# Kernel optimization log

Hardware: AMD Instinct MI355X
Metric: run time of the kernel (lower is better)

## Reference

```python
import jax, jax.numpy as jnp
import numpy as np

B = 131072
IN_CH, SEQ = 16, 5
EMB = 64
UDIM = 16
E = 16
RANK = 8
NCLS = 10
TOPK = 2
NUSERS = 1000
EPS_LN = 1e-5


def _ln(x, g, b):
    mu = x.mean(-1, keepdims=True)
    var = ((x - mu) ** 2).mean(-1, keepdims=True)
    return (x - mu) * jax.lax.rsqrt(var + EPS_LN) * g + b


def setup_inputs() -> dict:
    key = jax.random.key(0)
    ks = jax.random.split(key, 20)
    s = lambda i, shape, scale=0.05: (jax.random.normal(ks[i], shape, jnp.float32) * scale)
    return {
        "x": jax.random.normal(ks[0], (B, IN_CH, SEQ), jnp.float32),
        "user_ids": jax.random.randint(ks[1], (B,), 0, NUSERS),
        # backbone: fc1 (80->64), fc2 (64->64), LayerNorm
        "bb_w1": s(2, (IN_CH * SEQ, 64)), "bb_b1": jnp.zeros((64,), jnp.float32),
        "bb_w2": s(3, (64, EMB)), "bb_b2": jnp.zeros((EMB,), jnp.float32),
        "bb_g": jnp.ones((EMB,), jnp.float32), "bb_beta": jnp.zeros((EMB,), jnp.float32),
        # bilinear gate
        "gU": s(4, (E, EMB, RANK), 0.02), "gV": s(5, (E, UDIM, RANK), 0.02),
        "gb": jnp.zeros((E,), jnp.float32),
        # experts (stacked): fc1 (emb->emb), LN, fc2 (emb->ncls)
        "e_w1": s(6, (E, EMB, EMB)), "e_b1": jnp.zeros((E, EMB), jnp.float32),
        "e_g": jnp.ones((E, EMB), jnp.float32), "e_beta": jnp.zeros((E, EMB), jnp.float32),
        "e_w2": s(7, (E, EMB, NCLS)), "e_b2": jnp.zeros((E, NCLS), jnp.float32),
        # user embedding table
        "ut": s(8, (NUSERS, UDIM), 1.0),
    }


def reference(x, user_ids, bb_w1, bb_b1, bb_w2, bb_b2, bb_g, bb_beta,
              gU, gV, gb, e_w1, e_b1, e_g, e_beta, e_w2, e_b2, ut):
    gelu = lambda t: jax.nn.gelu(t, approximate=False)
    # backbone
    xf = x.reshape(x.shape[0], -1)                      # [B, 80]
    h = gelu(xf @ bb_w1 + bb_b1)
    h = gelu(h @ bb_w2 + bb_b2)
    h = _ln(h, bb_g, bb_beta)                           # [B, EMB]
    # user embedding lookup
    u = ut[user_ids]                                    # [B, UDIM]
    # bilinear gate
    hU = jnp.einsum('bd,edr->ber', h, gU)
    uV = jnp.einsum('bd,edr->ber', u, gV)
    g = (hU * uV).sum(-1) + gb                          # [B, E]
    w = jax.nn.softmax(g, axis=-1)
    if TOPK and TOPK < E:
        _, idx = jax.lax.top_k(w, TOPK)
        mask = jnp.zeros_like(w).at[jnp.arange(w.shape[0])[:, None], idx].set(1.0)
        wm = w * mask
        w = wm / jnp.maximum(wm.sum(-1, keepdims=True), 1e-9)
    # experts, dense over all E (matches torch stack over ModuleList)
    z = gelu(jnp.einsum('bd,edk->bek', h, e_w1) + e_b1)  # [B, E, EMB]
    z = _ln(z, e_g, e_beta)
    lpe = jnp.einsum('bek,ekc->bec', z, e_w2) + e_b2     # [B, E, NCLS]
    logits = jnp.einsum('be,bec->bc', w, lpe)            # [B, NCLS]
    return logits
```

## Files before the change

### kernel.cpp

```cpp
#include <hip/hip_runtime.h>
#include <math.h>

#define BATCH   131072
#define IN_F    80
#define EMB     64
#define NE      16
#define RANK    8
#define UDIM    16
#define NCLS    10
#define NUSERS  1000

#define OFF_H      0ull
#define OFF_A      33554432ull
#define OFF_TOPE   37650432ull
#define OFF_TOPW   38699008ull
#define OFF_PAIRB  39747584ull
#define OFF_PAIRW  40796160ull
#define OFF_HIST   41844736ull
#define OFF_OFFS   41845760ull
#define OFF_CUR    41846784ull

__device__ __forceinline__ float gelu_f(float v) {
    return 0.5f * v * (1.0f + erff(v * 0.70710678118654752440f));
}
__device__ __forceinline__ float4 gelu4(float4 v) {
    v.x = gelu_f(v.x); v.y = gelu_f(v.y); v.z = gelu_f(v.z); v.w = gelu_f(v.w);
    return v;
}
__device__ __forceinline__ float4 sfma4(float s, float4 w, float4 a) {
    a.x = fmaf(s, w.x, a.x); a.y = fmaf(s, w.y, a.y);
    a.z = fmaf(s, w.z, a.z); a.w = fmaf(s, w.w, a.w);
    return a;
}
__device__ __forceinline__ float4 ffma4(float4 v, float4 w, float4 a) {
    a.x = fmaf(v.x, w.x, a.x); a.y = fmaf(v.y, w.y, a.y);
    a.z = fmaf(v.z, w.z, a.z); a.w = fmaf(v.w, w.w, a.w);
    return a;
}
__device__ __forceinline__ float4 add4(float4 a, float4 b) {
    a.x += b.x; a.y += b.y; a.z += b.z; a.w += b.w; return a;
}
__device__ __forceinline__ float4 ln4(float4 z, float mu, float inv, float4 g, float4 bb) {
    float4 r;
    r.x = fmaf((z.x - mu) * inv, g.x, bb.x);
    r.y = fmaf((z.y - mu) * inv, g.y, bb.y);
    r.z = fmaf((z.z - mu) * inv, g.z, bb.z);
    r.w = fmaf((z.w - mu) * inv, g.w, bb.w);
    return r;
}
__device__ __forceinline__ float4 shflx4(float4 a, int m) {
    float4 r;
    r.x = __shfl_xor(a.x, m, 64); r.y = __shfl_xor(a.y, m, 64);
    r.z = __shfl_xor(a.z, m, 64); r.w = __shfl_xor(a.w, m, 64);
    return r;
}

#define FMA16Z(S, WB) do { \
    z0 = sfma4((S), (WB)[0],  z0); z1 = sfma4((S), (WB)[1],  z1); \
    z2 = sfma4((S), (WB)[2],  z2); z3 = sfma4((S), (WB)[3],  z3); \
    z4 = sfma4((S), (WB)[4],  z4); z5 = sfma4((S), (WB)[5],  z5); \
    z6 = sfma4((S), (WB)[6],  z6); z7 = sfma4((S), (WB)[7],  z7); \
    z8 = sfma4((S), (WB)[8],  z8); z9 = sfma4((S), (WB)[9],  z9); \
    za = sfma4((S), (WB)[10], za); zb = sfma4((S), (WB)[11], zb); \
    zc = sfma4((S), (WB)[12], zc); zd = sfma4((S), (WB)[13], zd); \
    ze = sfma4((S), (WB)[14], ze); zf = sfma4((S), (WB)[15], zf); } while (0)

__global__ void k_prep(const float* __restrict__ gU, const float* __restrict__ gV,
                       const float* __restrict__ ut, float* __restrict__ A)
{
    int idx = blockIdx.x * 256 + threadIdx.x;
    if (idx >= NUSERS * NE) return;
    int u = idx / NE, e = idx - u * NE;

    const float4* up = (const float4*)(ut + (size_t)u * UDIM);
    float4 u0 = up[0], u1 = up[1], u2 = up[2], u3 = up[3];

    float4 va = make_float4(0.f, 0.f, 0.f, 0.f);
    float4 vb = make_float4(0.f, 0.f, 0.f, 0.f);
    const float4* gv4 = (const float4*)gV;
#define UVSTEP(UD, DD) do { \
        float4 g0 = gv4[(e * UDIM + (DD)) * 2 + 0]; \
        float4 g1 = gv4[(e * UDIM + (DD)) * 2 + 1]; \
        va = sfma4((UD), g0, va); vb = sfma4((UD), g1, vb); } while (0)
    UVSTEP(u0.x, 0);  UVSTEP(u0.y, 1);  UVSTEP(u0.z, 2);  UVSTEP(u0.w, 3);
    UVSTEP(u1.x, 4);  UVSTEP(u1.y, 5);  UVSTEP(u1.z, 6);  UVSTEP(u1.w, 7);
    UVSTEP(u2.x, 8);  UVSTEP(u2.y, 9);  UVSTEP(u2.z, 10); UVSTEP(u2.w, 11);
    UVSTEP(u3.x, 12); UVSTEP(u3.y, 13); UVSTEP(u3.z, 14); UVSTEP(u3.w, 15);
#undef UVSTEP

    const float4* gu4 = (const float4*)gU;
    float* Ao = A + ((size_t)u * NE + e) * EMB;
    for (int d = 0; d < EMB; ++d) {
        float4 q0 = gu4[(e * EMB + d) * 2 + 0];
        float4 q1 = gu4[(e * EMB + d) * 2 + 1];
        float a = 0.0f;
        a = fmaf(q0.x, va.x, a); a = fmaf(q0.y, va.y, a);
        a = fmaf(q0.z, va.z, a); a = fmaf(q0.w, va.w, a);
        a = fmaf(q1.x, vb.x, a); a = fmaf(q1.y, vb.y, a);
        a = fmaf(q1.z, vb.z, a); a = fmaf(q1.w, vb.w, a);
        Ao[d] = a;
    }
}

__global__ __launch_bounds__(256) void k_fc1(
    const float* __restrict__ x,
    const float* __restrict__ w1, const float* __restrict__ b1,
    float* __restrict__ h1_out)
{
    __shared__ __align__(16) float4 s_w1[IN_F * 16];
    __shared__ __align__(16) float4 s_b1[16];

    const int tid = threadIdx.x;
    {
        const float4* g1 = (const float4*)w1;
        for (int i = tid; i < IN_F * 16; i += 256) s_w1[i] = g1[i];
        if (tid < 16) s_b1[tid] = ((const float4*)b1)[tid];
    }
    __syncthreads();

    const int b = blockIdx.x * 256 + tid;
    const float4* xp = (const float4*)(x + (size_t)b * IN_F);

    float4 z0 = s_b1[0],  z1 = s_b1[1],  z2 = s_b1[2],  z3 = s_b1[3];
    float4 z4 = s_b1[4],  z5 = s_b1[5],  z6 = s_b1[6],  z7 = s_b1[7];
    float4 z8 = s_b1[8],  z9 = s_b1[9],  za = s_b1[10], zb = s_b1[11];
    float4 zc = s_b1[12], zd = s_b1[13], ze = s_b1[14], zf = s_b1[15];

#pragma unroll 1
    for (int t = 0; t < 5; ++t) {
        float4 xA = xp[4*t+0], xB = xp[4*t+1], xC = xp[4*t+2], xD = xp[4*t+3];
        const float4* wr = s_w1 + (t * 16) * 16;
        FMA16Z(xA.x, wr);       FMA16Z(xA.y, wr + 16);  FMA16Z(xA.z, wr + 32);  FMA16Z(xA.w, wr + 48);
        FMA16Z(xB.x, wr + 64);  FMA16Z(xB.y, wr + 80);  FMA16Z(xB.z, wr + 96);  FMA16Z(xB.w, wr + 112);
        FMA16Z(xC.x, wr + 128); FMA16Z(xC.y, wr + 144); FMA16Z(xC.z, wr + 160); FMA16Z(xC.w, wr + 176);
        FMA16Z(xD.x, wr + 192); FMA16Z(xD.y, wr + 208); FMA16Z(xD.z, wr + 224); FMA16Z(xD.w, wr + 240);
    }
    z0 = gelu4(z0); z1 = gelu4(z1); z2 = gelu4(z2); z3 = gelu4(z3);
    z4 = gelu4(z4); z5 = gelu4(z5); z6 = gelu4(z6); z7 = gelu4(z7);
    z8 = gelu4(z8); z9 = gelu4(z9); za = gelu4(za); zb = gelu4(zb);
    zc = gelu4(zc); zd = gelu4(zd); ze = gelu4(ze); zf = gelu4(zf);

    float4* ho = (float4*)(h1_out + (size_t)b * EMB);
    ho[0] = z0;  ho[1] = z1;  ho[2] = z2;  ho[3] = z3;
    ho[4] = z4;  ho[5] = z5;  ho[6] = z6;  ho[7] = z7;
    ho[8] = z8;  ho[9] = z9;  ho[10] = za; ho[11] = zb;
    ho[12] = zc; ho[13] = zd; ho[14] = ze; ho[15] = zf;
}

__global__ __launch_bounds__(256) void k_fc2gate(
    float* h,
    const int* __restrict__ uid,
    const float* __restrict__ w2, const float* __restrict__ b2,
    const float* __restrict__ gam, const float* __restrict__ bet,
    const float* __restrict__ A, const float* __restrict__ gb,
    int* __restrict__ top_e, float* __restrict__ top_w, int* __restrict__ hist)
{
    __shared__ __align__(16) float4 s_w2[EMB * 16];
    __shared__ __align__(16) float4 s_b2[16], s_ga[16], s_be[16];
    __shared__ float s_gb[NE];
    __shared__ int s_hist[NE];

    const int tid = threadIdx.x;
    {
        const float4* g2 = (const float4*)w2;
        for (int i = tid; i < EMB * 16; i += 256) s_w2[i] = g2[i];
        if (tid < 16) {
            s_b2[tid] = ((const float4*)b2)[tid];
            s_ga[tid] = ((const float4*)gam)[tid];
            s_be[tid] = ((const float4*)bet)[tid];
        }
        if (tid < NE) { s_gb[tid] = gb[tid]; s_hist[tid] = 0; }
    }
    __syncthreads();

    const int b = blockIdx.x * 256 + tid;
    float4* hp = (float4*)(h + (size_t)b * EMB);

    float4 z0 = s_b2[0],  z1 = s_b2[1],  z2 = s_b2[2],  z3 = s_b2[3];
    float4 z4 = s_b2[4],  z5 = s_b2[5],  z6 = s_b2[6],  z7 = s_b2[7];
    float4 z8 = s_b2[8],  z9 = s_b2[9],  za = s_b2[10], zb = s_b2[11];
    float4 zc = s_b2[12], zd = s_b2[13], ze = s_b2[14], zf = s_b2[15];
#pragma unroll 1
    for (int t = 0; t < 4; ++t) {
        float4 hA = hp[4*t+0], hB = hp[4*t+1], hC = hp[4*t+2], hD = hp[4*t+3];
        const float4* wr = s_w2 + (t * 16) * 16;
        FMA16Z(hA.x, wr);       FMA16Z(hA.y, wr + 16);  FMA16Z(hA.z, wr + 32);  FMA16Z(hA.w, wr + 48);
        FMA16Z(hB.x, wr + 64);  FMA16Z(hB.y, wr + 80);  FMA16Z(hB.z, wr + 96);  FMA16Z(hB.w, wr + 112);
        FMA16Z(hC.x, wr + 128); FMA16Z(hC.y, wr + 144); FMA16Z(hC.z, wr + 160); FMA16Z(hC.w, wr + 176);
        FMA16Z(hD.x, wr + 192); FMA16Z(hD.y, wr + 208); FMA16Z(hD.z, wr + 224); FMA16Z(hD.w, wr + 240);
    }
    z0 = gelu4(z0); z1 = gelu4(z1); z2 = gelu4(z2); z3 = gelu4(z3);
    z4 = gelu4(z4); z5 = gelu4(z5); z6 = gelu4(z6); z7 = gelu4(z7);
    z8 = gelu4(z8); z9 = gelu4(z9); za = gelu4(za); zb = gelu4(zb);
    zc = gelu4(zc); zd = gelu4(zd); ze = gelu4(ze); zf = gelu4(zf);

    float4 sA = add4(add4(add4(z0, z1), add4(z2, z3)), add4(add4(z4, z5), add4(z6, z7)));
    float4 sB = add4(add4(add4(z8, z9), add4(za, zb)), add4(add4(zc, zd), add4(ze, zf)));
    float4 sS = add4(sA, sB);
    float mu = (sS.x + sS.y + sS.z + sS.w) * (1.0f / 64.0f);
    float4 vv = make_float4(0.f, 0.f, 0.f, 0.f);
#define BBV(Z) do { float4 d4; d4.x = (Z).x - mu; d4.y = (Z).y - mu; d4.z = (Z).z - mu; d4.w = (Z).w - mu; \
                    vv = ffma4(d4, d4, vv); } while (0)
    BBV(z0); BBV(z1); BBV(z2); BBV(z3); BBV(z4); BBV(z5); BBV(z6); BBV(z7);
    BBV(z8); BBV(z9); BBV(za); BBV(zb); BBV(zc); BBV(zd); BBV(ze); BBV(zf);
#undef BBV
    float var = (vv.x + vv.y + vv.z + vv.w) * (1.0f / 64.0f);
    float inv = 1.0f / sqrtf(var + 1e-5f);
    z0 = ln4(z0, mu, inv, s_ga[0],  s_be[0]);
    z1 = ln4(z1, mu, inv, s_ga[1],  s_be[1]);
    z2 = ln4(z2, mu, inv, s_ga[2],  s_be[2]);
    z3 = ln4(z3, mu, inv, s_ga[3],  s_be[3]);
    z4 = ln4(z4, mu, inv, s_ga[4],  s_be[4]);
    z5 = ln4(z5, mu, inv, s_ga[5],  s_be[5]);
    z6 = ln4(z6, mu, inv, s_ga[6],  s_be[6]);
    z7 = ln4(z7, mu, inv, s_ga[7],  s_be[7]);
    z8 = ln4(z8, mu, inv, s_ga[8],  s_be[8]);
    z9 = ln4(z9, mu, inv, s_ga[9],  s_be[9]);
    za = ln4(za, mu, inv, s_ga[10], s_be[10]);
    zb = ln4(zb, mu, inv, s_ga[11], s_be[11]);
    zc = ln4(zc, mu, inv, s_ga[12], s_be[12]);
    zd = ln4(zd, mu, inv, s_ga[13], s_be[13]);
    ze = ln4(ze, mu, inv, s_ga[14], s_be[14]);
    zf = ln4(zf, mu, inv, s_ga[15], s_be[15]);

    hp[0] = z0;  hp[1] = z1;  hp[2] = z2;  hp[3] = z3;
    hp[4] = z4;  hp[5] = z5;  hp[6] = z6;  hp[7] = z7;
    hp[8] = z8;  hp[9] = z9;  hp[10] = za; hp[11] = zb;
    hp[12] = zc; hp[13] = zd; hp[14] = ze; hp[15] = zf;

    const int u = uid[b];
    const float4* Ap = (const float4*)(A + (size_t)u * NE * EMB);
    float m0 = -1e30f, m1 = -1e30f;
    int i0 = 0, i1 = 0;
#pragma unroll 1
    for (int e = 0; e < NE; ++e) {
        const float4* ap = Ap + e * 16;
        float4 ac = make_float4(0.f, 0.f, 0.f, 0.f);
        ac = ffma4(z0, ap[0],  ac); ac = ffma4(z1, ap[1],  ac);
        ac = ffma4(z2, ap[2],  ac); ac = ffma4(z3, ap[3],  ac);
        ac = ffma4(z4, ap[4],  ac); ac = ffma4(z5, ap[5],  ac);
        ac = ffma4(z6, ap[6],  ac); ac = ffma4(z7, ap[7],  ac);
        ac = ffma4(z8, ap[8],  ac); ac = ffma4(z9, ap[9],  ac);
        ac = ffma4(za, ap[10], ac); ac = ffma4(zb, ap[11], ac);
        ac = ffma4(zc, ap[12], ac); ac = ffma4(zd, ap[13], ac);
        ac = ffma4(ze, ap[14], ac); ac = ffma4(zf, ap[15], ac);
        float ge = ((ac.x + ac.y) + (ac.z + ac.w)) + s_gb[e];
        if (ge > m0)      { m1 = m0; i1 = i0; m0 = ge; i0 = e; }
        else if (ge > m1) { m1 = ge; i1 = e; }
    }
    float t = expf(m1 - m0);
    float w0n = 1.0f / (1.0f + t);
    float w1n = t / (1.0f + t);

    top_e[2*b+0] = i0; top_w[2*b+0] = w0n;
    top_e[2*b+1] = i1; top_w[2*b+1] = w1n;
    atomicAdd(&s_hist[i0], 1);
    atomicAdd(&s_hist[i1], 1);
    __syncthreads();
    if (tid < NE) atomicAdd(&hist[tid], s_hist[tid]);
}

__global__ void k_scan(const int* __restrict__ hist, int* __restrict__ offs, int* __restrict__ cur)
{
    if (blockIdx.x == 0 && threadIdx.x == 0) {
        int acc = 0;
        for (int e = 0; e < NE; ++e) { offs[e] = acc; cur[e] = acc; acc += hist[e]; }
    }
}

__global__ __launch_bounds__(256) void k_scatter(
    const int* __restrict__ top_e, const float* __restrict__ top_w,
    int* __restrict__ cur, int* __restrict__ pair_b, float* __restrict__ pair_w)
{
    __shared__ int lh[NE];
    __shared__ int lbase[NE];
    const int tid = threadIdx.x;
    if (tid < NE) lh[tid] = 0;
    __syncthreads();

    const int b = blockIdx.x * 256 + tid;
    const int e0 = top_e[2*b+0];
    const int e1 = top_e[2*b+1];
    atomicAdd(&lh[e0], 1);
    atomicAdd(&lh[e1], 1);
    __syncthreads();
    if (tid < NE) {
        lbase[tid] = atomicAdd(&cur[tid], lh[tid]);
        lh[tid] = 0;
    }
    __syncthreads();
    int r0 = atomicAdd(&lh[e0], 1);
    int p0 = lbase[e0] + r0;
    pair_b[p0] = b; pair_w[p0] = top_w[2*b+0];
    int r1 = atomicAdd(&lh[e1], 1);
    int p1 = lbase[e1] + r1;
    pair_b[p1] = b; pair_w[p1] = top_w[2*b+1];
}

#define EXP_BX 128
__global__ __launch_bounds__(256, 2) void k_expert(
    const float* __restrict__ h,
    const int* __restrict__ pair_b, const float* __restrict__ pair_w,
    const int* __restrict__ hist, const int* __restrict__ offs,
    const float* __restrict__ ew1, const float* __restrict__ eb1,
    const float* __restrict__ eg, const float* __restrict__ ebeta,
    const float* __restrict__ ew2, const float* __restrict__ eb2,
    float* __restrict__ out)
{
    const int e = blockIdx.y;
    const int cnt = hist[e];
    if ((int)(blockIdx.x * 64) >= cnt) return;

    __shared__ __align__(16) float4 s_w1[EMB * 16];
    __shared__ __align__(16) float4 s_w2[EMB * 3];
    __shared__ __align__(16) float4 s_b1[16], s_ga[16], s_be[16], s_b2[3];

    const int tid = threadIdx.x;
    {
        const float4* g1 = (const float4*)(ew1 + (size_t)e * EMB * EMB);
        for (int i = tid; i < EMB * 16; i += 256) s_w1[i] = g1[i];
        float* w2f = (float*)s_w2;
        for (int i = tid; i < EMB * 12; i += 256) {
            int k = i / 12, c = i - k * 12;
            w2f[i] = (c < NCLS) ? ew2[((size_t)e * EMB + k) * NCLS + c] : 0.0f;
        }
        if (tid < 16) {
            s_b1[tid] = ((const float4*)(eb1   + (size_t)e * EMB))[tid];
            s_ga[tid] = ((const float4*)(eg    + (size_t)e * EMB))[tid];
            s_be[tid] = ((const float4*)(ebeta + (size_t)e * EMB))[tid];
        }
        float* b2f = (float*)s_b2;
        if (tid < 12) b2f[tid] = (tid < NCLS) ? eb2[e * NCLS + tid] : 0.0f;
    }
    __syncthreads();

    const int base = offs[e];
    const int q  = tid & 3;
    const int pl = tid >> 2;

    for (int p0 = blockIdx.x * 64; p0 < cnt; p0 += EXP_BX * 64) {
        const int pr = p0 + pl;
        if (pr >= cnt) continue;
        const int idx = base + pr;
        const int b = pair_b[idx];
        const float pw = pair_w[idx];

        const float4* hp = (const float4*)(h + (size_t)b * EMB);

        float4 z0 = s_b1[q*4+0], z1 = s_b1[q*4+1], z2 = s_b1[q*4+2], z3 = s_b1[q*4+3];
#define FMA4Q(S, WB) do { \
        z0 = sfma4((S), (WB)[0], z0); z1 = sfma4((S), (WB)[1], z1); \
        z2 = sfma4((S), (WB)[2], z2); z3 = sfma4((S), (WB)[3], z3); } while (0)
#pragma unroll 1
        for (int t = 0; t < 4; ++t) {
            float4 hA = hp[4*t+0], hB = hp[4*t+1], hC = hp[4*t+2], hD = hp[4*t+3];
            const float4* wr = s_w1 + (t * 16) * 16 + q * 4;
            FMA4Q(hA.x, wr + 0*16);  FMA4Q(hA.y, wr + 1*16);  FMA4Q(hA.z, wr + 2*16);  FMA4Q(hA.w, wr + 3*16);
            FMA4Q(hB.x, wr + 4*16);  FMA4Q(hB.y, wr + 5*16);  FMA4Q(hB.z, wr + 6*16);  FMA4Q(hB.w, wr + 7*16);
            FMA4Q(hC.x, wr + 8*16);  FMA4Q(hC.y, wr + 9*16);  FMA4Q(hC.z, wr + 10*16); FMA4Q(hC.w, wr + 11*16);
            FMA4Q(hD.x, wr + 12*16); FMA4Q(hD.y, wr + 13*16); FMA4Q(hD.z, wr + 14*16); FMA4Q(hD.w, wr + 15*16);
        }
#undef FMA4Q
        z0 = gelu4(z0); z1 = gelu4(z1); z2 = gelu4(z2); z3 = gelu4(z3);

        float4 sA = add4(add4(z0, z1), add4(z2, z3));
        float sl = (sA.x + sA.y) + (sA.z + sA.w);
        sl += __shfl_xor(sl, 1, 64);
        sl += __shfl_xor(sl, 2, 64);
        float mu = sl * (1.0f / 64.0f);

        float4 vv = make_float4(0.f, 0.f, 0.f, 0.f);
#define EXV(Z) do { float4 d4; d4.x = (Z).x - mu; d4.y = (Z).y - mu; d4.z = (Z).z - mu; d4.w = (Z).w - mu; \
                    vv = ffma4(d4, d4, vv); } while (0)
        EXV(z0); EXV(z1); EXV(z2); EXV(z3);
#undef EXV
        float vl = (vv.x + vv.y) + (vv.z + vv.w);
        vl += __shfl_xor(vl, 1, 64);
        vl += __shfl_xor(vl, 2, 64);
        float var = vl * (1.0f / 64.0f);
        float inv = 1.0f / sqrtf(var + 1e-5f);

        z0 = ln4(z0, mu, inv, s_ga[q*4+0], s_be[q*4+0]);
        z1 = ln4(z1, mu, inv, s_ga[q*4+1], s_be[q*4+1]);
        z2 = ln4(z2, mu, inv, s_ga[q*4+2], s_be[q*4+2]);
        z3 = ln4(z3, mu, inv, s_ga[q*4+3], s_be[q*4+3]);

        float4 a0 = make_float4(0.f, 0.f, 0.f, 0.f);
        float4 a1 = make_float4(0.f, 0.f, 0.f, 0.f);
        float4 a2 = make_float4(0.f, 0.f, 0.f, 0.f);
#define EXF2(S, I) do { \
        const float4* wr = s_w2 + (q * 16 + (I)) * 3; \
        a0 = sfma4((S), wr[0], a0); a1 = sfma4((S), wr[1], a1); a2 = sfma4((S), wr[2], a2); } while (0)
        EXF2(z0.x, 0);  EXF2(z0.y, 1);  EXF2(z0.z, 2);  EXF2(z0.w, 3);
        EXF2(z1.x, 4);  EXF2(z1.y, 5);  EXF2(z1.z, 6);  EXF2(z1.w, 7);
        EXF2(z2.x, 8);  EXF2(z2.y, 9);  EXF2(z2.z, 10); EXF2(z2.w, 11);
        EXF2(z3.x, 12); EXF2(z3.y, 13); EXF2(z3.z, 14); EXF2(z3.w, 15);
#undef EXF2

        a0 = add4(a0, shflx4(a0, 1)); a0 = add4(a0, shflx4(a0, 2));
        a1 = add4(a1, shflx4(a1, 1)); a1 = add4(a1, shflx4(a1, 2));
        a2 = add4(a2, shflx4(a2, 1)); a2 = add4(a2, shflx4(a2, 2));

        if (q == 0) {
            a0 = add4(a0, s_b2[0]); a1 = add4(a1, s_b2[1]); a2 = add4(a2, s_b2[2]);
            float* ob = out + (size_t)b * NCLS;
            atomicAdd(ob + 0, pw * a0.x);
            atomicAdd(ob + 1, pw * a0.y);
            atomicAdd(ob + 2, pw * a0.z);
            atomicAdd(ob + 3, pw * a0.w);
            atomicAdd(ob + 4, pw * a1.x);
            atomicAdd(ob + 5, pw * a1.y);
            atomicAdd(ob + 6, pw * a1.z);
            atomicAdd(ob + 7, pw * a1.w);
            atomicAdd(ob + 8, pw * a2.x);
            atomicAdd(ob + 9, pw * a2.y);
        }
    }
}

extern "C" void kernel_launch(void* const* d_in, const int* in_sizes, int n_in,
                              void* d_out, int out_size, void* d_ws, size_t ws_size,
                              hipStream_t stream)
{
    (void)in_sizes; (void)n_in; (void)out_size; (void)ws_size;

    const float* x     = (const float*)d_in[0];
    const int*   uid   = (const int*)  d_in[1];
    const float* bb_w1 = (const float*)d_in[2];
    const float* bb_b1 = (const float*)d_in[3];
    const float* bb_w2 = (const float*)d_in[4];
    const float* bb_b2 = (const float*)d_in[5];
    const float* bb_g  = (const float*)d_in[6];
    const float* bb_be = (const float*)d_in[7];
    const float* gU    = (const float*)d_in[8];
    const float* gV    = (const float*)d_in[9];
    const float* gb    = (const float*)d_in[10];
    const float* e_w1  = (const float*)d_in[11];
    const float* e_b1  = (const float*)d_in[12];
    const float* e_g   = (const float*)d_in[13];
    const float* e_be  = (const float*)d_in[14];
    const float* e_w2  = (const float*)d_in[15];
    const float* e_b2  = (const float*)d_in[16];
    const float* ut    = (const float*)d_in[17];

    float* out = (float*)d_out;
    char*  ws  = (char*)d_ws;

    float* h      = (float*)(ws + OFF_H);
    float* A      = (float*)(ws + OFF_A);
    int*   top_e  = (int*)  (ws + OFF_TOPE);
    float* top_w  = (float*)(ws + OFF_TOPW);
    int*   pair_b = (int*)  (ws + OFF_PAIRB);
    float* pair_w = (float*)(ws + OFF_PAIRW);
    int*   hist   = (int*)  (ws + OFF_HIST);
    int*   offs   = (int*)  (ws + OFF_OFFS);
    int*   cur    = (int*)  (ws + OFF_CUR);

    hipMemsetAsync(out, 0, (size_t)BATCH * NCLS * sizeof(float), stream);
    hipMemsetAsync(hist, 0, NE * sizeof(int), stream);

    k_prep<<<(NUSERS * NE + 255) / 256, 256, 0, stream>>>(gU, gV, ut, A);
    k_fc1<<<BATCH / 256, 256, 0, stream>>>(x, bb_w1, bb_b1, h);
    k_fc2gate<<<BATCH / 256, 256, 0, stream>>>(h, uid, bb_w2, bb_b2, bb_g, bb_be,
                                               A, gb, top_e, top_w, hist);
    k_scan<<<1, 64, 0, stream>>>(hist, offs, cur);
    k_scatter<<<BATCH / 256, 256, 0, stream>>>(top_e, top_w, cur, pair_b, pair_w);
    dim3 eg(EXP_BX, NE);
    k_expert<<<eg, 256, 0, stream>>>(h, pair_b, pair_w, hist, offs,
                                     e_w1, e_b1, e_g, e_be, e_w2, e_b2, out);
}
```

Before: 384.3 us.

## Split rows across 4 lanes with 2 rows per thread in fc1, fc2gate, expert

Restructures the backbone fc1 and fc2+gate kernels so each group of four lanes shares two batch rows, with each lane computing a quarter of the output columns. LayerNorm statistics and the gate dot products are reduced with shuffles. The expert kernel now processes two pairs per lane group and uses a padded per-quarter w2 layout in shared memory. The aim is lower register pressure, so that two blocks fit per CU, and reuse of each shared-memory weight load across two rows. The cost is extra shuffle reductions and redundant per-row loads of h/x across lanes.

```diff
diff --git a/kernel.cpp b/kernel.cpp
--- a/kernel.cpp
+++ b/kernel.cpp
@@ -55,15 +55,13 @@
     return r;
 }
 
-#define FMA16Z(S, WB) do { \
-    z0 = sfma4((S), (WB)[0],  z0); z1 = sfma4((S), (WB)[1],  z1); \
-    z2 = sfma4((S), (WB)[2],  z2); z3 = sfma4((S), (WB)[3],  z3); \
-    z4 = sfma4((S), (WB)[4],  z4); z5 = sfma4((S), (WB)[5],  z5); \
-    z6 = sfma4((S), (WB)[6],  z6); z7 = sfma4((S), (WB)[7],  z7); \
-    z8 = sfma4((S), (WB)[8],  z8); z9 = sfma4((S), (WB)[9],  z9); \
-    za = sfma4((S), (WB)[10], za); zb = sfma4((S), (WB)[11], zb); \
-    zc = sfma4((S), (WB)[12], zc); zd = sfma4((S), (WB)[13], zd); \
-    ze = sfma4((S), (WB)[14], ze); zf = sfma4((S), (WB)[15], zf); } while (0)
+#define FMAD2(SA, SB) do { \
+    float4 w0_ = wr[0], w1_ = wr[1], w2_ = wr[2], w3_ = wr[3]; \
+    zA0 = sfma4((SA), w0_, zA0); zA1 = sfma4((SA), w1_, zA1); \
+    zA2 = sfma4((SA), w2_, zA2); zA3 = sfma4((SA), w3_, zA3); \
+    zB0 = sfma4((SB), w0_, zB0); zB1 = sfma4((SB), w1_, zB1); \
+    zB2 = sfma4((SB), w2_, zB2); zB3 = sfma4((SB), w3_, zB3); \
+    wr += 16; } while (0)
 
 __global__ void k_prep(const float* __restrict__ gU, const float* __restrict__ gV,
                        const float* __restrict__ ut, float* __restrict__ A)
@@ -102,7 +100,7 @@
     }
 }
 
-__global__ __launch_bounds__(256) void k_fc1(
+__global__ __launch_bounds__(256, 2) void k_fc1(
     const float* __restrict__ x,
     const float* __restrict__ w1, const float* __restrict__ b1,
     float* __restrict__ h1_out)
@@ -118,36 +116,34 @@
     }
     __syncthreads();
 
-    const int b = blockIdx.x * 256 + tid;
-    const float4* xp = (const float4*)(x + (size_t)b * IN_F);
-
-    float4 z0 = s_b1[0],  z1 = s_b1[1],  z2 = s_b1[2],  z3 = s_b1[3];
-    float4 z4 = s_b1[4],  z5 = s_b1[5],  z6 = s_b1[6],  z7 = s_b1[7];
-    float4 z8 = s_b1[8],  z9 = s_b1[9],  za = s_b1[10], zb = s_b1[11];
-    float4 zc = s_b1[12], zd = s_b1[13], ze = s_b1[14], zf = s_b1[15];
+    const int q  = tid & 3;
+    const int pl = tid >> 2;
+    const int bA = blockIdx.x * 128 + 2 * pl;
+    const int bB = bA + 1;
+    const float4* xpA = (const float4*)(x + (size_t)bA * IN_F);
+    const float4* xpB = (const float4*)(x + (size_t)bB * IN_F);
+
+    float4 zA0 = s_b1[q*4+0], zA1 = s_b1[q*4+1], zA2 = s_b1[q*4+2], zA3 = s_b1[q*4+3];
+    float4 zB0 = zA0, zB1 = zA1, zB2 = zA2, zB3 = zA3;
 
 #pragma unroll 1
-    for (int t = 0; t < 5; ++t) {
-        float4 xA = xp[4*t+0], xB = xp[4*t+1], xC = xp[4*t+2], xD = xp[4*t+3];
-        const float4* wr = s_w1 + (t * 16) * 16;
-        FMA16Z(xA.x, wr);       FMA16Z(xA.y, wr + 16);  FMA16Z(xA.z, wr + 32);  FMA16Z(xA.w, wr + 48);
-        FMA16Z(xB.x, wr + 64);  FMA16Z(xB.y, wr + 80);  FMA16Z(xB.z, wr + 96);  FMA16Z(xB.w, wr + 112);
-        FMA16Z(xC.x, wr + 128); FMA16Z(xC.y, wr + 144); FMA16Z(xC.z, wr + 160); FMA16Z(xC.w, wr + 176);
-        FMA16Z(xD.x, wr + 192); FMA16Z(xD.y, wr + 208); FMA16Z(xD.z, wr + 224); FMA16Z(xD.w, wr + 240);
-    }
-    z0 = gelu4(z0); z1 = gelu4(z1); z2 = gelu4(z2); z3 = gelu4(z3);
-    z4 = gelu4(z4); z5 = gelu4(z5); z6 = gelu4(z6); z7 = gelu4(z7);
-    z8 = gelu4(z8); z9 = gelu4(z9); za = gelu4(za); zb = gelu4(zb);
-    zc = gelu4(zc); zd = gelu4(zd); ze = gelu4(ze); zf = gelu4(zf);
-
-    float4* ho = (float4*)(h1_out + (size_t)b * EMB);
-    ho[0] = z0;  ho[1] = z1;  ho[2] = z2;  ho[3] = z3;
-    ho[4] = z4;  ho[5] = z5;  ho[6] = z6;  ho[7] = z7;
-    ho[8] = z8;  ho[9] = z9;  ho[10] = za; ho[11] = zb;
-    ho[12] = zc; ho[13] = zd; ho[14] = ze; ho[15] = zf;
-}
-
-__global__ __launch_bounds__(256) void k_fc2gate(
+    for (int t = 0; t < 10; ++t) {
+        float4 a0 = xpA[2*t+0], a1 = xpA[2*t+1];
+        float4 b0 = xpB[2*t+0], b1 = xpB[2*t+1];
+        const float4* wr = s_w1 + (8*t) * 16 + q * 4;
+        FMAD2(a0.x, b0.x); FMAD2(a0.y, b0.y); FMAD2(a0.z, b0.z); FMAD2(a0.w, b0.w);
+        FMAD2(a1.x, b1.x); FMAD2(a1.y, b1.y); FMAD2(a1.z, b1.z); FMAD2(a1.w, b1.w);
+    }
+    zA0 = gelu4(zA0); zA1 = gelu4(zA1); zA2 = gelu4(zA2); zA3 = gelu4(zA3);
+    zB0 = gelu4(zB0); zB1 = gelu4(zB1); zB2 = gelu4(zB2); zB3 = gelu4(zB3);
+
+    float4* hoA = (float4*)(h1_out + (size_t)bA * EMB);
+    float4* hoB = (float4*)(h1_out + (size_t)bB * EMB);
+    hoA[q*4+0] = zA0; hoA[q*4+1] = zA1; hoA[q*4+2] = zA2; hoA[q*4+3] = zA3;
+    hoB[q*4+0] = zB0; hoB[q*4+1] = zB1; hoB[q*4+2] = zB2; hoB[q*4+3] = zB3;
+}
+
+__global__ __launch_bounds__(256, 2) void k_fc2gate(
     float* h,
     const int* __restrict__ uid,
     const float* __restrict__ w2, const float* __restrict__ b2,
@@ -173,89 +169,119 @@
     }
     __syncthreads();
 
-    const int b = blockIdx.x * 256 + tid;
-    float4* hp = (float4*)(h + (size_t)b * EMB);
-
-    float4 z0 = s_b2[0],  z1 = s_b2[1],  z2 = s_b2[2],  z3 = s_b2[3];
-    float4 z4 = s_b2[4],  z5 = s_b2[5],  z6 = s_b2[6],  z7 = s_b2[7];
-    float4 z8 = s_b2[8],  z9 = s_b2[9],  za = s_b2[10], zb = s_b2[11];
-    float4 zc = s_b2[12], zd = s_b2[13], ze = s_b2[14], zf = s_b2[15];
+    const int q  = tid & 3;
+    const int pl = tid >> 2;
+    const int bA = blockIdx.x * 128 + 2 * pl;
+    const int bB = bA + 1;
+    float4* hpA = (float4*)(h + (size_t)bA * EMB);
+    float4* hpB = (float4*)(h + (size_t)bB * EMB);
+
+    float4 zA0 = s_b2[q*4+0], zA1 = s_b2[q*4+1], zA2 = s_b2[q*4+2], zA3 = s_b2[q*4+3];
+    float4 zB0 = zA0, zB1 = zA1, zB2 = zA2, zB3 = zA3;
+
 #pragma unroll 1
-    for (int t = 0; t < 4; ++t) {
-        float4 hA = hp[4*t+0], hB = hp[4*t+1], hC = hp[4*t+2], hD = hp[4*t+3];
-        const float4* wr = s_w2 + (t * 16) * 16;
-        FMA16Z(hA.x, wr);       FMA16Z(hA.y, wr + 16);  FMA16Z(hA.z, wr + 32);  FMA16Z(hA.w, wr + 48);
-        FMA16Z(hB.x, wr + 64);  FMA16Z(hB.y, wr + 80);  FMA16Z(hB.z, wr + 96);  FMA16Z(hB.w, wr + 112);
-        FMA16Z(hC.x, wr + 128); FMA16Z(hC.y, wr + 144); FMA16Z(hC.z, wr + 160); FMA16Z(hC.w, wr + 176);
-        FMA16Z(hD.x, wr + 192); FMA16Z(hD.y, wr + 208); FMA16Z(hD.z, wr + 224); FMA16Z(hD.w, wr + 240);
-    }
-    z0 = gelu4(z0); z1 = gelu4(z1); z2 = gelu4(z2); z3 = gelu4(z3);
-    z4 = gelu4(z4); z5 = gelu4(z5); z6 = gelu4(z6); z7 = gelu4(z7);
-    z8 = gelu4(z8); z9 = gelu4(z9); za = gelu4(za); zb = gelu4(zb);
-    zc = gelu4(zc); zd = gelu4(zd); ze = gelu4(ze); zf = gelu4(zf);
-
-    float4 sA = add4(add4(add4(z0, z1), add4(z2, z3)), add4(add4(z4, z5), add4(z6, z7)));
-    float4 sB = add4(add4(add4(z8, z9), add4(za, zb)), add4(add4(zc, zd), add4(ze, zf)));
-    float4 sS = add4(sA, sB);
-    float mu = (sS.x + sS.y + sS.z + sS.w) * (1.0f / 64.0f);
-    float4 vv = make_float4(0.f, 0.f, 0.f, 0.f);
-#define BBV(Z) do { float4 d4; d4.x = (Z).x - mu; d4.y = (Z).y - mu; d4.z = (Z).z - mu; d4.w = (Z).w - mu; \
-                    vv = ffma4(d4, d4, vv); } while (0)
-    BBV(z0); BBV(z1); BBV(z2); BBV(z3); BBV(z4); BBV(z5); BBV(z6); BBV(z7);
-    BBV(z8); BBV(z9); BBV(za); BBV(zb); BBV(zc); BBV(zd); BBV(ze); BBV(zf);
-#undef BBV
-    float var = (vv.x + vv.y + vv.z + vv.w) * (1.0f / 64.0f);
-    float inv = 1.0f / sqrtf(var + 1e-5f);
-    z0 = ln4(z0, mu, inv, s_ga[0],  s_be[0]);
-    z1 = ln4(z1, mu, inv, s_ga[1],  s_be[1]);
-    z2 = ln4(z2, mu, inv, s_ga[2],  s_be[2]);
-    z3 = ln4(z3, mu, inv, s_ga[3],  s_be[3]);
-    z4 = ln4(z4, mu, inv, s_ga[4],  s_be[4]);
-    z5 = ln4(z5, mu, inv, s_ga[5],  s_be[5]);
-    z6 = ln4(z6, mu, inv, s_ga[6],  s_be[6]);
-    z7 = ln4(z7, mu, inv, s_ga[7],  s_be[7]);
-    z8 = ln4(z8, mu, inv, s_ga[8],  s_be[8]);
-    z9 = ln4(z9, mu, inv, s_ga[9],  s_be[9]);
-    za = ln4(za, mu, inv, s_ga[10], s_be[10]);
-    zb = ln4(zb, mu, inv, s_ga[11], s_be[11]);
-    zc = ln4(zc, mu, inv, s_ga[12], s_be[12]);
-    zd = ln4(zd, mu, inv, s_ga[13], s_be[13]);
-    ze = ln4(ze, mu, inv, s_ga[14], s_be[14]);
-    zf = ln4(zf, mu, inv, s_ga[15], s_be[15]);
-
-    hp[0] = z0;  hp[1] = z1;  hp[2] = z2;  hp[3] = z3;
-    hp[4] = z4;  hp[5] = z5;  hp[6] = z6;  hp[7] = z7;
-    hp[8] = z8;  hp[9] = z9;  hp[10] = za; hp[11] = zb;
-    hp[12] = zc; hp[13] = zd; hp[14] = ze; hp[15] = zf;
-
-    const int u = uid[b];
-    const float4* Ap = (const float4*)(A + (size_t)u * NE * EMB);
-    float m0 = -1e30f, m1 = -1e30f;
-    int i0 = 0, i1 = 0;
-#pragma unroll 1
-    for (int e = 0; e < NE; ++e) {
-        const float4* ap = Ap + e * 16;
-        float4 ac = make_float4(0.f, 0.f, 0.f, 0.f);
-        ac = ffma4(z0, ap[0],  ac); ac = ffma4(z1, ap[1],  ac);
-        ac = ffma4(z2, ap[2],  ac); ac = ffma4(z3, ap[3],  ac);
-        ac = ffma4(z4, ap[4],  ac); ac = ffma4(z5, ap[5],  ac);
-        ac = ffma4(z6, ap[6],  ac); ac = ffma4(z7, ap[7],  ac);
-        ac = ffma4(z8, ap[8],  ac); ac = ffma4(z9, ap[9],  ac);
-        ac = ffma4(za, ap[10], ac); ac = ffma4(zb, ap[11], ac);
-        ac = ffma4(zc, ap[12], ac); ac = ffma4(zd, ap[13], ac);
-        ac = ffma4(ze, ap[14], ac); ac = ffma4(zf, ap[15], ac);
-        float ge = ((ac.x + ac.y) + (ac.z + ac.w)) + s_gb[e];
-        if (ge > m0)      { m1 = m0; i1 = i0; m0 = ge; i0 = e; }
-        else if (ge > m1) { m1 = ge; i1 = e; }
-    }
-    float t = expf(m1 - m0);
-    float w0n = 1.0f / (1.0f + t);
-    float w1n = t / (1.0f + t);
-
-    top_e[2*b+0] = i0; top_w[2*b+0] = w0n;
-    top_e[2*b+1] = i1; top_w[2*b+1] = w1n;
-    atomicAdd(&s_hist[i0], 1);
-    atomicAdd(&s_hist[i1], 1);
+    for (int t = 0; t < 8; ++t) {
+        float4 a0 = hpA[2*t+0], a1 = hpA[2*t+1];
+        float4 b0 = hpB[2*t+0], b1 = hpB[2*t+1];
+        const float4* wr = s_w2 + (8*t) * 16 + q * 4;
+        FMAD2(a0.x, b0.x); FMAD2(a0.y, b0.y); FMAD2(a0.z, b0.z); FMAD2(a0.w, b0.w);
+        FMAD2(a1.x, b1.x); FMAD2(a1.y, b1.y); FMAD2(a1.z, b1.z); FMAD2(a1.w, b1.w);
+    }
+    zA0 = gelu4(zA0); zA1 = gelu4(zA1); zA2 = gelu4(zA2); zA3 = gelu4(zA3);
+    zB0 = gelu4(zB0); zB1 = gelu4(zB1); zB2 = gelu4(zB2); zB3 = gelu4(zB3);
+
+    float4 sA4 = add4(add4(zA0, zA1), add4(zA2, zA3));
+    float slA = (sA4.x + sA4.y) + (sA4.z + sA4.w);
+    slA += __shfl_xor(slA, 1, 64); slA += __shfl_xor(slA, 2, 64);
+    float muA = slA * (1.0f / 64.0f);
+    float4 sB4 = add4(add4(zB0, zB1), add4(zB2, zB3));
+    float slB = (sB4.x + sB4.y) + (sB4.z + sB4.w);
+    slB += __shfl_xor(slB, 1, 64); slB += __shfl_xor(slB, 2, 64);
+    float muB = slB * (1.0f / 64.0f);
+
+    float4 vvA = make_float4(0.f, 0.f, 0.f, 0.f);
+    float4 vvB = make_float4(0.f, 0.f, 0.f, 0.f);
+#define VACC(V, Z, MU) do { float4 d4; d4.x = (Z).x - (MU); d4.y = (Z).y - (MU); \
+        d4.z = (Z).z - (MU); d4.w = (Z).w - (MU); V = ffma4(d4, d4, V); } while (0)
+    VACC(vvA, zA0, muA); VACC(vvA, zA1, muA); VACC(vvA, zA2, muA); VACC(vvA, zA3, muA);
+    VACC(vvB, zB0, muB); VACC(vvB, zB1, muB); VACC(vvB, zB2, muB); VACC(vvB, zB3, muB);
+#undef VACC
+    float vlA = (vvA.x + vvA.y) + (vvA.z + vvA.w);
+    vlA += __shfl_xor(vlA, 1, 64); vlA += __shfl_xor(vlA, 2, 64);
+    float invA = 1.0f / sqrtf(vlA * (1.0f / 64.0f) + 1e-5f);
+    float vlB = (vvB.x + vvB.y) + (vvB.z + vvB.w);
+    vlB += __shfl_xor(vlB, 1, 64); vlB += __shfl_xor(vlB, 2, 64);
+    float invB = 1.0f / sqrtf(vlB * (1.0f / 64.0f) + 1e-5f);
+
+    zA0 = ln4(zA0, muA, invA, s_ga[q*4+0], s_be[q*4+0]);
+    zA1 = ln4(zA1, muA, invA, s_ga[q*4+1], s_be[q*4+1]);
+    zA2 = ln4(zA2, muA, invA, s_ga[q*4+2], s_be[q*4+2]);
+    zA3 = ln4(zA3, muA, invA, s_ga[q*4+3], s_be[q*4+3]);
+    zB0 = ln4(zB0, muB, invB, s_ga[q*4+0], s_be[q*4+0]);
+    zB1 = ln4(zB1, muB, invB, s_ga[q*4+1], s_be[q*4+1]);
+    zB2 = ln4(zB2, muB, invB, s_ga[q*4+2], s_be[q*4+2]);
+    zB3 = ln4(zB3, muB, invB, s_ga[q*4+3], s_be[q*4+3]);
+
+    hpA[q*4+0] = zA0; hpA[q*4+1] = zA1; hpA[q*4+2] = zA2; hpA[q*4+3] = zA3;
+    hpB[q*4+0] = zB0; hpB[q*4+1] = zB1; hpB[q*4+2] = zB2; hpB[q*4+3] = zB3;
+
+    const int uA = uid[bA], uB = uid[bB];
+    const float* AbA = A + (size_t)uA * NE * EMB + q * 16;
+    const float* AbB = A + (size_t)uB * NE * EMB + q * 16;
+    float gA0,gA1,gA2,gA3,gA4,gA5,gA6,gA7,gA8,gA9,gAa,gAb,gAc,gAd,gAe,gAf;
+    float gB0,gB1,gB2,gB3,gB4,gB5,gB6,gB7,gB8,gB9,gBa,gBb,gBc,gBd,gBe,gBf;
+#define GDOT(GV, AB, E, Z0, Z1, Z2, Z3) do { \
+    const float4* ap = (const float4*)((AB) + (E) * EMB); \
+    float4 ac = make_float4(0.f, 0.f, 0.f, 0.f); \
+    ac = ffma4(Z0, ap[0], ac); ac = ffma4(Z1, ap[1], ac); \
+    ac = ffma4(Z2, ap[2], ac); ac = ffma4(Z3, ap[3], ac); \
+    GV = (ac.x + ac.y) + (ac.z + ac.w); \
+    GV += __shfl_xor(GV, 1, 64); GV += __shfl_xor(GV, 2, 64); \
+    GV += s_gb[(E)]; } while (0)
+    GDOT(gA0, AbA, 0,  zA0,zA1,zA2,zA3); GDOT(gA1, AbA, 1,  zA0,zA1,zA2,zA3);
+    GDOT(gA2, AbA, 2,  zA0,zA1,zA2,zA3); GDOT(gA3, AbA, 3,  zA0,zA1,zA2,zA3);
+    GDOT(gA4, AbA, 4,  zA0,zA1,zA2,zA3); GDOT(gA5, AbA, 5,  zA0,zA1,zA2,zA3);
+    GDOT(gA6, AbA, 6,  zA0,zA1,zA2,zA3); GDOT(gA7, AbA, 7,  zA0,zA1,zA2,zA3);
+    GDOT(gA8, AbA, 8,  zA0,zA1,zA2,zA3); GDOT(gA9, AbA, 9,  zA0,zA1,zA2,zA3);
+    GDOT(gAa, AbA, 10, zA0,zA1,zA2,zA3); GDOT(gAb, AbA, 11, zA0,zA1,zA2,zA3);
+    GDOT(gAc, AbA, 12, zA0,zA1,zA2,zA3); GDOT(gAd, AbA, 13, zA0,zA1,zA2,zA3);
+    GDOT(gAe, AbA, 14, zA0,zA1,zA2,zA3); GDOT(gAf, AbA, 15, zA0,zA1,zA2,zA3);
+    GDOT(gB0, AbB, 0,  zB0,zB1,zB2,zB3); GDOT(gB1, AbB, 1,  zB0,zB1,zB2,zB3);
+    GDOT(gB2, AbB, 2,  zB0,zB1,zB2,zB3); GDOT(gB3, AbB, 3,  zB0,zB1,zB2,zB3);
+    GDOT(gB4, AbB, 4,  zB0,zB1,zB2,zB3); GDOT(gB5, AbB, 5,  zB0,zB1,zB2,zB3);
+    GDOT(gB6, AbB, 6,  zB0,zB1,zB2,zB3); GDOT(gB7, AbB, 7,  zB0,zB1,zB2,zB3);
+    GDOT(gB8, AbB, 8,  zB0,zB1,zB2,zB3); GDOT(gB9, AbB, 9,  zB0,zB1,zB2,zB3);
+    GDOT(gBa, AbB, 10, zB0,zB1,zB2,zB3); GDOT(gBb, AbB, 11, zB0,zB1,zB2,zB3);
+    GDOT(gBc, AbB, 12, zB0,zB1,zB2,zB3); GDOT(gBd, AbB, 13, zB0,zB1,zB2,zB3);
+    GDOT(gBe, AbB, 14, zB0,zB1,zB2,zB3); GDOT(gBf, AbB, 15, zB0,zB1,zB2,zB3);
+#undef GDOT
+
+#define T2(G, E) do { float gv_ = (G); \
+    if (gv_ > m0) { m1 = m0; i1 = i0; m0 = gv_; i0 = (E); } \
+    else if (gv_ > m1) { m1 = gv_; i1 = (E); } } while (0)
+    if (q == 0) {
+        {
+            float m0 = -1e30f, m1 = -1e30f; int i0 = 0, i1 = 0;
+            T2(gA0,0); T2(gA1,1); T2(gA2,2); T2(gA3,3); T2(gA4,4); T2(gA5,5);
+            T2(gA6,6); T2(gA7,7); T2(gA8,8); T2(gA9,9); T2(gAa,10); T2(gAb,11);
+            T2(gAc,12); T2(gAd,13); T2(gAe,14); T2(gAf,15);
+            float t = expf(m1 - m0);
+            top_e[2*bA+0] = i0; top_w[2*bA+0] = 1.0f / (1.0f + t);
+            top_e[2*bA+1] = i1; top_w[2*bA+1] = t / (1.0f + t);
+            atomicAdd(&s_hist[i0], 1); atomicAdd(&s_hist[i1], 1);
+        }
+        {
+            float m0 = -1e30f, m1 = -1e30f; int i0 = 0, i1 = 0;
+            T2(gB0,0); T2(gB1,1); T2(gB2,2); T2(gB3,3); T2(gB4,4); T2(gB5,5);
+            T2(gB6,6); T2(gB7,7); T2(gB8,8); T2(gB9,9); T2(gBa,10); T2(gBb,11);
+            T2(gBc,12); T2(gBd,13); T2(gBe,14); T2(gBf,15);
+            float t = expf(m1 - m0);
+            top_e[2*bB+0] = i0; top_w[2*bB+0] = 1.0f / (1.0f + t);
+            top_e[2*bB+1] = i1; top_w[2*bB+1] = t / (1.0f + t);
+            atomicAdd(&s_hist[i0], 1); atomicAdd(&s_hist[i1], 1);
+        }
+    }
+#undef T2
     __syncthreads();
     if (tid < NE) atomicAdd(&hist[tid], s_hist[tid]);
 }
@@ -309,111 +335,141 @@
 {
     const int e = blockIdx.y;
     const int cnt = hist[e];
-    if ((int)(blockIdx.x * 64) >= cnt) return;
+    if ((int)(blockIdx.x * 128) >= cnt) return;
 
     __shared__ __align__(16) float4 s_w1[EMB * 16];
-    __shared__ __align__(16) float4 s_w2[EMB * 3];
-    __shared__ __align__(16) float4 s_b1[16], s_ga[16], s_be[16], s_b2[3];
+    __shared__ __align__(16) float4 s_w2q[4 * 52];
+    __shared__ __align__(16) float4 s_b1[16], s_ga[16], s_be[16];
+    __shared__ float s_b2s[12];
 
     const int tid = threadIdx.x;
     {
         const float4* g1 = (const float4*)(ew1 + (size_t)e * EMB * EMB);
         for (int i = tid; i < EMB * 16; i += 256) s_w1[i] = g1[i];
-        float* w2f = (float*)s_w2;
-        for (int i = tid; i < EMB * 12; i += 256) {
-            int k = i / 12, c = i - k * 12;
-            w2f[i] = (c < NCLS) ? ew2[((size_t)e * EMB + k) * NCLS + c] : 0.0f;
+        float* w2f = (float*)s_w2q;
+        for (int i = tid; i < 4 * 192; i += 256) {
+            int cp = i / 192, r = i - cp * 192;
+            int k = r / 12, c = r - k * 12;
+            w2f[cp * 208 + r] = (c < NCLS)
+                ? ew2[((size_t)e * EMB + cp * 16 + k) * NCLS + c] : 0.0f;
         }
         if (tid < 16) {
             s_b1[tid] = ((const float4*)(eb1   + (size_t)e * EMB))[tid];
             s_ga[tid] = ((const float4*)(eg    + (size_t)e * EMB))[tid];
             s_be[tid] = ((const float4*)(ebeta + (size_t)e * EMB))[tid];
         }
-        float* b2f = (float*)s_b2;
-        if (tid < 12) b2f[tid] = (tid < NCLS) ? eb2[e * NCLS + tid] : 0.0f;
+        if (tid < 12) s_b2s[tid] = (tid < NCLS) ? eb2[e * NCLS + tid] : 0.0f;
     }
     __syncthreads();
 
     const int base = offs[e];
     const int q  = tid & 3;
     const int pl = tid >> 2;
-
-    for (int p0 = blockIdx.x * 64; p0 < cnt; p0 += EXP_BX * 64) {
-        const int pr = p0 + pl;
-        if (pr >= cnt) continue;
-        const int idx = base + pr;
-        const int b = pair_b[idx];
-        const float pw = pair_w[idx];
-
-        const float4* hp = (const float4*)(h + (size_t)b * EMB);
-
-        float4 z0 = s_b1[q*4+0], z1 = s_b1[q*4+1], z2 = s_b1[q*4+2], z3 = s_b1[q*4+3];
-#define FMA4Q(S, WB) do { \
-        z0 = sfma4((S), (WB)[0], z0); z1 = sfma4((S), (WB)[1], z1); \
-        z2 = sfma4((S), (WB)[2], z2); z3 = sfma4((S), (WB)[3], z3); } while (0)
+    const float4* w2r = s_w2q + q * 52;
+
+    for (int p0 = blockIdx.x * 128; p0 < cnt; p0 += EXP_BX * 128) {
+        const int prA = p0 + 2 * pl;
+        if (prA >= cnt) continue;
+        const int prB = prA + 1;
+        const bool vB = (prB < cnt);
+        const int idxA = base + prA;
+        const int idxB = base + (vB ? prB : prA);
+        const int bA = pair_b[idxA], bB = pair_b[idxB];
+        const float pwA = pair_w[idxA], pwB = pair_w[idxB];
+
+        const float4* hpA = (const float4*)(h + (size_t)bA * EMB);
+        const float4* hpB = (const float4*)(h + (size_t)bB * EMB);
+
+        float4 zA0 = s_b1[q*4+0], zA1 = s_b1[q*4+1], zA2 = s_b1[q*4+2], zA3 = s_b1[q*4+3];
+        float4 zB0 = zA0, zB1 = zA1, zB2 = zA2, zB3 = zA3;
 #pragma unroll 1
-        for (int t = 0; t < 4; ++t) {
-            float4 hA = hp[4*t+0], hB = hp[4*t+1], hC = hp[4*t+2], hD = hp[4*t+3];
-            const float4* wr = s_w1 + (t * 16) * 16 + q * 4;
-            FMA4Q(hA.x, wr + 0*16);  FMA4Q(hA.y, wr + 1*16);  FMA4Q(hA.z, wr + 2*16);  FMA4Q(hA.w, wr + 3*16);
-            FMA4Q(hB.x, wr + 4*16);  FMA4Q(hB.y, wr + 5*16);  FMA4Q(hB.z, wr + 6*16);  FMA4Q(hB.w, wr + 7*16);
-            FMA4Q(hC.x, wr + 8*16);  FMA4Q(hC.y, wr + 9*16);  FMA4Q(hC.z, wr + 10*16); FMA4Q(hC.w, wr + 11*16);
-            FMA4Q(hD.x, wr + 12*16); FMA4Q(hD.y, wr + 13*16); FMA4Q(hD.z, wr + 14*16); FMA4Q(hD.w, wr + 15*16);
-        }
-#undef FMA4Q
-        z0 = gelu4(z0); z1 = gelu4(z1); z2 = gelu4(z2); z3 = gelu4(z3);
-
-        float4 sA = add4(add4(z0, z1), add4(z2, z3));
-        float sl = (sA.x + sA.y) + (sA.z + sA.w);
-        sl += __shfl_xor(sl, 1, 64);
-        sl += __shfl_xor(sl, 2, 64);
-        float mu = sl * (1.0f / 64.0f);
-
-        float4 vv = make_float4(0.f, 0.f, 0.f, 0.f);
-#define EXV(Z) do { float4 d4; d4.x = (Z).x - mu; d4.y = (Z).y - mu; d4.z = (Z).z - mu; d4.w = (Z).w - mu; \
-                    vv = ffma4(d4, d4, vv); } while (0)
-        EXV(z0); EXV(z1); EXV(z2); EXV(z3);
-#undef EXV
-        float vl = (vv.x + vv.y) + (vv.z + vv.w);
-        vl += __shfl_xor(vl, 1, 64);
-        vl += __shfl_xor(vl, 2, 64);
-        float var = vl * (1.0f / 64.0f);
-        float inv = 1.0f / sqrtf(var + 1e-5f);
-
-        z0 = ln4(z0, mu, inv, s_ga[q*4+0], s_be[q*4+0]);
-        z1 = ln4(z1, mu, inv, s_ga[q*4+1], s_be[q*4+1]);
-        z2 = ln4(z2, mu, inv, s_ga[q*4+2], s_be[q*4+2]);
-        z3 = ln4(z3, mu, inv, s_ga[q*4+3], s_be[q*4+3]);
-
-        float4 a0 = make_float4(0.f, 0.f, 0.f, 0.f);
-        float4 a1 = make_float4(0.f, 0.f, 0.f, 0.f);
-        float4 a2 = make_float4(0.f, 0.f, 0.f, 0.f);
-#define EXF2(S, I) do { \
-        const float4* wr = s_w2 + (q * 16 + (I)) * 3; \
-        a0 = sfma4((S), wr[0], a0); a1 = sfma4((S), wr[1], a1); a2 = sfma4((S), wr[2], a2); } while (0)
-        EXF2(z0.x, 0);  EXF2(z0.y, 1);  EXF2(z0.z, 2);  EXF2(z0.w, 3);
-        EXF2(z1.x, 4);  EXF2(z1.y, 5);  EXF2(z1.z, 6);  EXF2(z1.w, 7);
-        EXF2(z2.x, 8);  EXF2(z2.y, 9);  EXF2(z2.z, 10); EXF2(z2.w, 11);
-        EXF2(z3.x, 12); EXF2(z3.y, 13); EXF2(z3.z, 14); EXF2(z3.w, 15);
-#undef EXF2
-
-        a0 = add4(a0, shflx4(a0, 1)); a0 = add4(a0, shflx4(a0, 2));
-        a1 = add4(a1, shflx4(a1, 1)); a1 = add4(a1, shflx4(a1, 2));
-        a2 = add4(a2, shflx4(a2, 1)); a2 = add4(a2, shflx4(a2, 2));
+        for (int t = 0; t < 8; ++t) {
+            float4 a0 = hpA[2*t+0], a1 = hpA[2*t+1];
+            float4 b0 = hpB[2*t+0], b1 = hpB[2*t+1];
+            const float4* wr = s_w1 + (8*t) * 16 + q * 4;
+            FMAD2(a0.x, b0.x); FMAD2(a0.y, b0.y); FMAD2(a0.z, b0.z); FMAD2(a0.w, b0.w);
+            FMAD2(a1.x, b1.x); FMAD2(a1.y, b1.y); FMAD2(a1.z, b1.z); FMAD2(a1.w, b1.w);
+        }
+        zA0 = gelu4(zA0); zA1 = gelu4(zA1); zA2 = gelu4(zA2); zA3 = gelu4(zA3);
+        zB0 = gelu4(zB0); zB1 = gelu4(zB1); zB2 = gelu4(zB2); zB3 = gelu4(zB3);
+
+        float4 sA4 = add4(add4(zA0, zA1), add4(zA2, zA3));
+        float slA = (sA4.x + sA4.y) + (sA4.z + sA4.w);
+        slA += __shfl_xor(slA, 1, 64); slA += __shfl_xor(slA, 2, 64);
+        float muA = slA * (1.0f / 64.0f);
+        float4 sB4 = add4(add4(zB0, zB1), add4(zB2, zB3));
+        float slB = (sB4.x + sB4.y) + (sB4.z + sB4.w);
+        slB += __shfl_xor(slB, 1, 64); slB += __shfl_xor(slB, 2, 64);
+        float muB = slB * (1.0f / 64.0f);
+
+        float4 vvA = make_float4(0.f, 0.f, 0.f, 0.f);
+        float4 vvB = make_float4(0.f, 0.f, 0.f, 0.f);
+#define VACC(V, Z, MU) do { float4 d4; d4.x = (Z).x - (MU); d4.y = (Z).y - (MU); \
+        d4.z = (Z).z - (MU); d4.w = (Z).w - (MU); V = ffma4(d4, d4, V); } while (0)
+        VACC(vvA, zA0, muA); VACC(vvA, zA1, muA); VACC(vvA, zA2, muA); VACC(vvA, zA3, muA);
+        VACC(vvB, zB0, muB); VACC(vvB, zB1, muB); VACC(vvB, zB2, muB); VACC(vvB, zB3, muB);
+#undef VACC
+        float vlA = (vvA.x + vvA.y) + (vvA.z + vvA.w);
+        vlA += __shfl_xor(vlA, 1, 64); vlA += __shfl_xor(vlA, 2, 64);
+        float invA = 1.0f / sqrtf(vlA * (1.0f / 64.0f) + 1e-5f);
+        float vlB = (vvB.x + vvB.y) + (vvB.z + vvB.w);
+        vlB += __shfl_xor(vlB, 1, 64); vlB += __shfl_xor(vlB, 2, 64);
+        float invB = 1.0f / sqrtf(vlB * (1.0f / 64.0f) + 1e-5f);
+
+        zA0 = ln4(zA0, muA, invA, s_ga[q*4+0], s_be[q*4+0]);
+        zA1 = ln4(zA1, muA, invA, s_ga[q*4+1], s_be[q*4+1]);
+        zA2 = ln4(zA2, muA, invA, s_ga[q*4+2], s_be[q*4+2]);
+        zA3 = ln4(zA3, muA, invA, s_ga[q*4+3], s_be[q*4+3]);
+        zB0 = ln4(zB0, muB, invB, s_ga[q*4+0], s_be[q*4+0]);
+        zB1 = ln4(zB1, muB, invB, s_ga[q*4+1], s_be[q*4+1]);
+        zB2 = ln4(zB2, muB, invB, s_ga[q*4+2], s_be[q*4+2]);
+        zB3 = ln4(zB3, muB, invB, s_ga[q*4+3], s_be[q*4+3]);
+
+        float4 aA0 = make_float4(0.f,0.f,0.f,0.f), aA1 = aA0, aA2 = aA0;
+        float4 aB0 = aA0, aB1 = aA0, aB2 = aA0;
+#define EXF2D(ZA, ZB, I) do { \
+        const float4* wr2 = w2r + (I) * 3; \
+        float4 w0_ = wr2[0], w1_ = wr2[1], w2_ = wr2[2]; \
+        aA0 = sfma4((ZA), w0_, aA0); aA1 = sfma4((ZA), w1_, aA1); aA2 = sfma4((ZA), w2_, aA2); \
+        aB0 = sfma4((ZB), w0_, aB0); aB1 = sfma4((ZB), w1_, aB1); aB2 = sfma4((ZB), w2_, aB2); } while (0)
+        EXF2D(zA0.x, zB0.x, 0);  EXF2D(zA0.y, zB0.y, 1);  EXF2D(zA0.z, zB0.z, 2);  EXF2D(zA0.w, zB0.w, 3);
+        EXF2D(zA1.x, zB1.x, 4);  EXF2D(zA1.y, zB1.y, 5);  EXF2D(zA1.z, zB1.z, 6);  EXF2D(zA1.w, zB1.w, 7);
+        EXF2D(zA2.x, zB2.x, 8);  EXF2D(zA2.y, zB2.y, 9);  EXF2D(zA2.z, zB2.z, 10); EXF2D(zA2.w, zB2.w, 11);
+        EXF2D(zA3.x, zB3.x, 12); EXF2D(zA3.y, zB3.y, 13); EXF2D(zA3.z, zB3.z, 14); EXF2D(zA3.w, zB3.w, 15);
+#undef EXF2D
+
+        aA0 = add4(aA0, shflx4(aA0, 1)); aA0 = add4(aA0, shflx4(aA0, 2));
+        aA1 = add4(aA1, shflx4(aA1, 1)); aA1 = add4(aA1, shflx4(aA1, 2));
+        aA2 = add4(aA2, shflx4(aA2, 1)); aA2 = add4(aA2, shflx4(aA2, 2));
+        aB0 = add4(aB0, shflx4(aB0, 1)); aB0 = add4(aB0, shflx4(aB0, 2));
+        aB1 = add4(aB1, shflx4(aB1, 1)); aB1 = add4(aB1, shflx4(aB1, 2));
+        aB2 = add4(aB2, shflx4(aB2, 1)); aB2 = add4(aB2, shflx4(aB2, 2));
 
         if (q == 0) {
-            a0 = add4(a0, s_b2[0]); a1 = add4(a1, s_b2[1]); a2 = add4(a2, s_b2[2]);
-            float* ob = out + (size_t)b * NCLS;
-            atomicAdd(ob + 0, pw * a0.x);
-            atomicAdd(ob + 1, pw * a0.y);
-            atomicAdd(ob + 2, pw * a0.z);
-            atomicAdd(ob + 3, pw * a0.w);
-            atomicAdd(ob + 4, pw * a1.x);
-            atomicAdd(ob + 5, pw * a1.y);
-            atomicAdd(ob + 6, pw * a1.z);
-            atomicAdd(ob + 7, pw * a1.w);
-            atomicAdd(ob + 8, pw * a2.x);
-            atomicAdd(ob + 9, pw * a2.y);
+            float* obA = out + (size_t)bA * NCLS;
+            atomicAdd(obA + 0, pwA * (aA0.x + s_b2s[0]));
+            atomicAdd(obA + 1, pwA * (aA0.y + s_b2s[1]));
+            atomicAdd(obA + 2, pwA * (aA0.z + s_b2s[2]));
+            atomicAdd(obA + 3, pwA * (aA0.w + s_b2s[3]));
+            atomicAdd(obA + 4, pwA * (aA1.x + s_b2s[4]));
+            atomicAdd(obA + 5, pwA * (aA1.y + s_b2s[5]));
+            atomicAdd(obA + 6, pwA * (aA1.z + s_b2s[6]));
+            atomicAdd(obA + 7, pwA * (aA1.w + s_b2s[7]));
+            atomicAdd(obA + 8, pwA * (aA2.x + s_b2s[8]));
+            atomicAdd(obA + 9, pwA * (aA2.y + s_b2s[9]));
+            if (vB) {
+                float* obB = out + (size_t)bB * NCLS;
+                atomicAdd(obB + 0, pwB * (aB0.x + s_b2s[0]));
+                atomicAdd(obB + 1, pwB * (aB0.y + s_b2s[1]));
+                atomicAdd(obB + 2, pwB * (aB0.z + s_b2s[2]));
+                atomicAdd(obB + 3, pwB * (aB0.w + s_b2s[3]));
+                atomicAdd(obB + 4, pwB * (aB1.x + s_b2s[4]));
+                atomicAdd(obB + 5, pwB * (aB1.y + s_b2s[5]));
+                atomicAdd(obB + 6, pwB * (aB1.z + s_b2s[6]));
+                atomicAdd(obB + 7, pwB * (aB1.w + s_b2s[7]));
+                atomicAdd(obB + 8, pwB * (aB2.x + s_b2s[8]));
+                atomicAdd(obB + 9, pwB * (aB2.y + s_b2s[9]));
+            }
         }
     }
 }
@@ -460,8 +516,8 @@
     hipMemsetAsync(hist, 0, NE * sizeof(int), stream);
 
     k_prep<<<(NUSERS * NE + 255) / 256, 256, 0, stream>>>(gU, gV, ut, A);
-    k_fc1<<<BATCH / 256, 256, 0, stream>>>(x, bb_w1, bb_b1, h);
-    k_fc2gate<<<BATCH / 256, 256, 0, stream>>>(h, uid, bb_w2, bb_b2, bb_g, bb_be,
+    k_fc1<<<BATCH / 128, 256, 0, stream>>>(x, bb_w1, bb_b1, h);
+    k_fc2gate<<<BATCH / 128, 256, 0, stream>>>(h, uid, bb_w2, bb_b2, bb_g, bb_be,
                                                A, gb, top_e, top_w, hist);
     k_scan<<<1, 64, 0, stream>>>(hist, offs, cur);
     k_scatter<<<BATCH / 256, 256, 0, stream>>>(top_e, top_w, cur, pair_b, pair_w);
```

After: 308.9 us, median of 2. 1.24x faster.
